# Performance work log

Measured on AMD Instinct MI355X. Metric: run time of the kernel, lower is better.

The kernel has to match this reference:

```python
import jax, jax.numpy as jnp
import numpy as np

FEATURE_MAPS = [8, 4, 2, 1]
BOXES_PER_LOC = [4, 6, 6, 4]
IMAGE_SIZE = 128
DECODED_SIZE = 64
Z_WHAT = 64
CHANNELS = [64, 256, 128, 64, 32, 16, 3]  # conv-transpose pyramid 1x1 -> 64x64
BATCH = 4
EMPTY_CONST = -1000.0
N_LOC = sum(f * f for f in FEATURE_MAPS)            # 85
N_BOX = sum(f * f * b for f, b in zip(FEATURE_MAPS, BOXES_PER_LOC))  # 380


def _recon_indices():
    # Decoder.reconstruction_indices: expand per-location latents to per-box.
    idx, last = [], 0
    for fm, bpl in zip(FEATURE_MAPS, BOXES_PER_LOC):
        for i in range(fm * fm):
            idx.append(np.full(bpl, last + i, dtype=np.int32))
        last += fm * fm
    return np.concatenate(idx)


def setup_inputs() -> dict:
    key = jax.random.key(0)
    ks = jax.random.split(key, 16)
    inp = {
        'z_what': jax.random.normal(ks[0], (BATCH, N_LOC, Z_WHAT), jnp.float32),
        'z_where': jax.random.uniform(ks[1], (BATCH, N_BOX, 4), jnp.float32),
        'z_present': jax.random.randint(ks[2], (BATCH, N_BOX, 1), 0, 2).astype(jnp.int32),
        'z_depth': jax.random.normal(ks[3], (BATCH, N_LOC, 1), jnp.float32),
    }
    for i, (cin, cout) in enumerate(zip(CHANNELS[:-1], CHANNELS[1:])):
        inp[f'w{i}'] = jax.random.normal(ks[4 + i], (2, 2, cin, cout), jnp.float32) / np.sqrt(4.0 * cin)
        inp[f'b{i}'] = jnp.zeros((cout,), jnp.float32)
    return inp


def _what_decoder(z_flat, params):
    # (N, Z) -> (N, 3, 64, 64): stack of stride-2 kernel-2 conv transposes.
    x = z_flat[:, :, None, None]
    n = len(params)
    for i, (w, b) in enumerate(params):
        x = jax.lax.conv_transpose(x, w, strides=(2, 2), padding='VALID',
                                   dimension_numbers=('NCHW', 'HWIO', 'NCHW'))
        x = x + b[None, :, None, None]
        x = jax.nn.sigmoid(x) if i == n - 1 else jax.nn.relu(x)
    return x


def _sample_bilinear(img, px, py):
    # img (3, D, D); px/py (S,) pixel coords along cols/rows; zero outside.
    D = DECODED_SIZE
    x0 = jnp.floor(px)
    y0 = jnp.floor(py)
    wx = px - x0
    wy = py - y0

    def gather(yi, xi):
        vy = (yi >= 0) & (yi <= D - 1)
        vx = (xi >= 0) & (xi <= D - 1)
        yc = jnp.clip(yi.astype(jnp.int32), 0, D - 1)
        xc = jnp.clip(xi.astype(jnp.int32), 0, D - 1)
        vals = img[:, yc[:, None], xc[None, :]]  # (3, S, S)
        return vals * (vy[:, None] & vx[None, :]).astype(img.dtype)

    g00 = gather(y0, x0)
    g01 = gather(y0, x0 + 1)
    g10 = gather(y0 + 1, x0)
    g11 = gather(y0 + 1, x0 + 1)
    wyc = wy[None, :, None]
    wxc = wx[None, None, :]
    return (g00 * (1 - wyc) * (1 - wxc) + g01 * (1 - wyc) * wxc
            + g10 * wyc * (1 - wxc) + g11 * wyc * wxc)


def _where_stn(imgs, z_where):
    # Paste each decoded glyph into an IMAGE_SIZE canvas at box (cx, cy, w, h).
    S, D = IMAGE_SIZE, DECODED_SIZE
    cx, cy, w, h = (z_where[:, i] for i in range(4))
    sx = jnp.maximum(w, 1e-5)
    sy = jnp.maximum(h, 1e-5)
    out = jnp.linspace(-1.0, 1.0, S)
    xin = (out[None, :] - (2 * cx - 1)[:, None]) / sx[:, None]  # (N, S)
    yin = (out[None, :] - (2 * cy - 1)[:, None]) / sy[:, None]
    px = (xin + 1) * (D - 1) / 2
    py = (yin + 1) * (D - 1) / 2
    return jax.vmap(_sample_bilinear)(imgs, px, py)  # (N, 3, S, S)


def reference(z_what, z_where, z_present, z_depth, w0, b0, w1, b1, w2, b2, w3, b3, w4, b4, w5, b5):
    params = [(w0, b0), (w1, b1), (w2, b2), (w3, b3), (w4, b4), (w5, b5)]
    idx = jnp.asarray(_recon_indices())
    zw = jnp.take(z_what, idx, axis=1)   # (B, N_BOX, Z)
    zd = jnp.take(z_depth, idx, axis=1)  # (B, N_BOX, 1)
    B = zw.shape[0]
    decoded = _what_decoder(zw.reshape(B * N_BOX, Z_WHAT), params)
    transformed = _where_stn(decoded, z_where.reshape(B * N_BOX, 4))
    recon = transformed.reshape(B, N_BOX, 3, IMAGE_SIZE, IMAGE_SIZE)
    depths = jnp.where(z_present[..., 0] == 1, zd[..., 0], EMPTY_CONST)  # (B, N_BOX)
    weights = jax.nn.softmax(depths, axis=1)
    return jnp.einsum('bn,bnchw->bchw', weights, recon)
```

## Files before the change

kernel.cpp:

```cpp
#include <hip/hip_runtime.h>
#include <hip/hip_bf16.h>

#define NBOX  380
#define NLOCS 85
#define NINST 340
#define SPLIT 2

__device__ __forceinline__ int loc_of_box(int n) {
    if (n < 256) return n >> 2;
    if (n < 352) return 64 + (n - 256) / 6;
    if (n < 376) return 80 + (n - 352) / 6;
    return 84;
}

__device__ void box_params_dev(int b, const float* __restrict__ zwhere,
    const int* __restrict__ zpresent, const float* __restrict__ zdepth,
    float* wgt, float* sxs, float* oxs, float* sys, float* oys,
    int* binst, int* rect, int* cidx, int* cnt, float* sm)
{
    float* sd  = sm;
    float* red = sm + 384;
    const int tid = threadIdx.x;

    if (tid < NBOX) {
        int loc = loc_of_box(tid);
        sd[tid] = (zpresent[b * NBOX + tid] == 1) ? zdepth[b * NLOCS + loc] : -1000.0f;
    }
    __syncthreads();

    float m = (tid < NBOX) ? sd[tid] : -1e30f;
    red[tid] = m; __syncthreads();
    for (int s = 256; s > 0; s >>= 1) {
        if (tid < s) red[tid] = fmaxf(red[tid], red[tid + s]);
        __syncthreads();
    }
    m = red[0]; __syncthreads();

    float sum = (tid < NBOX) ? expf(sd[tid] - m) : 0.f;
    red[tid] = sum; __syncthreads();
    for (int s = 256; s > 0; s >>= 1) {
        if (tid < s) red[tid] += red[tid + s];
        __syncthreads();
    }
    float inv = 1.0f / red[0];
    __syncthreads();

    if (tid < NBOX) {
        int g = b * NBOX + tid;
        float wv = expf(sd[tid] - m) * inv;
        wgt[g] = wv;
        float cx = zwhere[g * 4 + 0], cy = zwhere[g * 4 + 1];
        float w  = zwhere[g * 4 + 2], h  = zwhere[g * 4 + 3];
        float isx = 1.0f / fmaxf(w, 1e-5f);
        float isy = 1.0f / fmaxf(h, 1e-5f);
        float sxv = isx * (63.0f / 127.0f);
        float oxv = 31.5f * (1.0f - 2.0f * cx * isx);
        float syv = isy * (63.0f / 127.0f);
        float oyv = 31.5f * (1.0f - 2.0f * cy * isy);
        sxs[g] = sxv; oxs[g] = oxv; sys[g] = syv; oys[g] = oyv;
        binst[g] = b * NLOCS + loc_of_box(tid);
        int wlo = min(127, max(0, (int)floorf((-1.0f - oxv) / sxv)));
        int whi = max(0, min(127, (int)ceilf((64.0f - oxv) / sxv)));
        int hlo = min(127, max(0, (int)floorf((-1.0f - oyv) / syv)));
        int hhi = max(0, min(127, (int)ceilf((64.0f - oyv) / syv)));
        rect[g] = wlo | (whi << 8) | (hlo << 16) | (hhi << 24);
        sd[tid] = wv;
    }
    __syncthreads();

    if (tid < 64) {
        int base = 0;
        for (int c = 0; c < 6; ++c) {
            int n = c * 64 + tid;
            bool p = (n < NBOX) && (sd[n] > 0.0f);
            unsigned long long mask = __ballot(p);
            int pos = __popcll(mask & ((1ull << tid) - 1ull));
            if (p) cidx[b * NBOX + base + pos] = n;
            base += __popcll(mask);
        }
        if (tid == 0) cnt[b] = base;
    }
}

__global__ __launch_bounds__(512, 2) void decode_fused_k(
    const float* __restrict__ z_what,
    const float* __restrict__ W0, const float* __restrict__ B0,
    const float* __restrict__ W1, const float* __restrict__ B1,
    const float* __restrict__ W2, const float* __restrict__ B2,
    const float* __restrict__ W3, const float* __restrict__ B3,
    const float* __restrict__ W4, const float* __restrict__ B4,
    const float* __restrict__ W5, const float* __restrict__ B5,
    const float* __restrict__ z_where, const int* __restrict__ z_present,
    const float* __restrict__ z_depth,
    float* __restrict__ wgt, float* __restrict__ sxs, float* __restrict__ oxs,
    float* __restrict__ sys, float* __restrict__ oys, int* __restrict__ binst,
    int* __restrict__ rect, int* __restrict__ cidx, int* __restrict__ cnt,
    float* __restrict__ dec)
{
    __shared__ __align__(16) float sm[13312];

    const int bid = blockIdx.x;
    if (bid >= SPLIT * NINST) {
        box_params_dev(bid - SPLIT * NINST, z_where, z_present, z_depth,
                       wgt, sxs, oxs, sys, oys, binst, rect, cidx, cnt, sm);
        return;
    }
    const int s    = bid / NINST;
    const int inst = bid - s * NINST;

    float* s_x = sm;
    float* aL0 = sm + 64;
    float* aL1 = sm + 576;
    float* aL2 = sm + 1600;
    float* aL4 = sm;
    float* aL3 = sm + 8704;

    const int tid = threadIdx.x;

    if (tid < 64) s_x[tid] = z_what[inst * 64 + tid];
    __syncthreads();

    {
        const int c0 = tid & 255;
        const int j0 = tid >> 8;
        const int ft = 3 - (2 * s + j0);
        const float* wp = W0 + (size_t)ft * 64 * 256 + c0;
        float a = 0.f;
        #pragma unroll 8
        for (int k = 0; k < 64; ++k)
            a = fmaf(s_x[k], wp[k * 256], a);
        aL0[j0 * 256 + c0] = fmaxf(a + B0[c0], 0.f);
    }
    __syncthreads();

    {
        const int c1 = tid & 127;
        const int x1 = tid >> 7;
        const int j = x1 >> 1, dj = x1 & 1;
        const float* wA = W1 + (size_t)(3 - dj) * 256 * 128 + c1;
        const float* wB = W1 + (size_t)(1 - dj) * 256 * 128 + c1;
        const float* xp = aL0 + j * 256;
        float a0 = 0.f, a1 = 0.f;
        #pragma unroll 4
        for (int q = 0; q < 64; ++q) {
            float4 xq = *(const float4*)&xp[q * 4];
            a0 = fmaf(xq.x, wA[(q*4+0)*128], a0); a1 = fmaf(xq.x, wB[(q*4+0)*128], a1);
            a0 = fmaf(xq.y, wA[(q*4+1)*128], a0); a1 = fmaf(xq.y, wB[(q*4+1)*128], a1);
            a0 = fmaf(xq.z, wA[(q*4+2)*128], a0); a1 = fmaf(xq.z, wB[(q*4+2)*128], a1);
            a0 = fmaf(xq.w, wA[(q*4+3)*128], a0); a1 = fmaf(xq.w, wB[(q*4+3)*128], a1);
        }
        float bb = B1[c1];
        aL1[(0 * 4 + x1) * 128 + c1] = fmaxf(a0 + bb, 0.f);
        aL1[(1 * 4 + x1) * 128 + c1] = fmaxf(a1 + bb, 0.f);
    }
    __syncthreads();

    {
        const int c2 = tid & 63;
        const int x2 = tid >> 6;
        const int j = x2 >> 1, dj = x2 & 1;
        const float* wA = W2 + (size_t)(3 - dj) * 128 * 64 + c2;
        const float* wB = W2 + (size_t)(1 - dj) * 128 * 64 + c2;
        const float* xp0 = aL1 + (0 * 4 + j) * 128;
        const float* xp1 = aL1 + (1 * 4 + j) * 128;
        float a00 = 0.f, a01 = 0.f, a10 = 0.f, a11 = 0.f;
        #pragma unroll 4
        for (int q = 0; q < 32; ++q) {
            float4 x0 = *(const float4*)&xp0[q * 4];
            float4 x1 = *(const float4*)&xp1[q * 4];
            #pragma unroll
            for (int kk = 0; kk < 4; ++kk) {
                int k = q * 4 + kk;
                float xa = (kk==0)?x0.x:(kk==1)?x0.y:(kk==2)?x0.z:x0.w;
                float xb = (kk==0)?x1.x:(kk==1)?x1.y:(kk==2)?x1.z:x1.w;
                float wa = wA[k * 64], wb = wB[k * 64];
                a00 = fmaf(xa, wa, a00); a01 = fmaf(xa, wb, a01);
                a10 = fmaf(xb, wa, a10); a11 = fmaf(xb, wb, a11);
            }
        }
        float bb = B2[c2];
        aL2[(0 * 8 + x2) * 64 + c2] = fmaxf(a00 + bb, 0.f);
        aL2[(1 * 8 + x2) * 64 + c2] = fmaxf(a01 + bb, 0.f);
        aL2[(2 * 8 + x2) * 64 + c2] = fmaxf(a10 + bb, 0.f);
        aL2[(3 * 8 + x2) * 64 + c2] = fmaxf(a11 + bb, 0.f);
    }
    __syncthreads();

    {
        const int c3 = tid & 31;
        const int x3 = tid >> 5;
        const int j = x3 >> 1, dj = x3 & 1;
        const float* wA = W3 + (size_t)(3 - dj) * 64 * 32 + c3;
        const float* wB = W3 + (size_t)(1 - dj) * 64 * 32 + c3;
        float accA[4], accB[4];
        #pragma unroll
        for (int il = 0; il < 4; ++il) { accA[il] = 0.f; accB[il] = 0.f; }
        #pragma unroll
        for (int q = 0; q < 16; ++q) {
            float4 xr[4];
            #pragma unroll
            for (int il = 0; il < 4; ++il)
                xr[il] = *(const float4*)&aL2[(il * 8 + j) * 64 + q * 4];
            #pragma unroll
            for (int kk = 0; kk < 4; ++kk) {
                int k = q * 4 + kk;
                float wa = wA[k * 32], wb = wB[k * 32];
                #pragma unroll
                for (int il = 0; il < 4; ++il) {
                    float xv = (kk==0)?xr[il].x:(kk==1)?xr[il].y:(kk==2)?xr[il].z:xr[il].w;
                    accA[il] = fmaf(xv, wa, accA[il]);
                    accB[il] = fmaf(xv, wb, accB[il]);
                }
            }
        }
        float bb = B3[c3];
        #pragma unroll
        for (int il = 0; il < 4; ++il) {
            aL3[((2 * il + 0) * 16 + x3) * 36 + c3] = fmaxf(accA[il] + bb, 0.f);
            aL3[((2 * il + 1) * 16 + x3) * 36 + c3] = fmaxf(accB[il] + bb, 0.f);
        }
    }
    __syncthreads();

    {
        const int c4 = tid & 15;
        const int x4 = tid >> 4;
        const int j = x4 >> 1, dj = x4 & 1;
        const float* wA = W4 + (size_t)(3 - dj) * 32 * 16 + c4;
        const float* wB = W4 + (size_t)(1 - dj) * 32 * 16 + c4;
        float accA[8], accB[8];
        #pragma unroll
        for (int il = 0; il < 8; ++il) { accA[il] = 0.f; accB[il] = 0.f; }
        #pragma unroll
        for (int q = 0; q < 8; ++q) {
            float4 xr[8];
            #pragma unroll
            for (int il = 0; il < 8; ++il)
                xr[il] = *(const float4*)&aL3[(il * 16 + j) * 36 + q * 4];
            #pragma unroll
            for (int kk = 0; kk < 4; ++kk) {
                int k = q * 4 + kk;
                float wa = wA[k * 16], wb = wB[k * 16];
                #pragma unroll
                for (int il = 0; il < 8; ++il) {
                    float xv = (kk==0)?xr[il].x:(kk==1)?xr[il].y:(kk==2)?xr[il].z:xr[il].w;
                    accA[il] = fmaf(xv, wa, accA[il]);
                    accB[il] = fmaf(xv, wb, accB[il]);
                }
            }
        }
        float bb = B4[c4];
        #pragma unroll
        for (int il = 0; il < 8; ++il) {
            aL4[((2 * il + 0) * 32 + x4) * 17 + c4] = fmaxf(accA[il] + bb, 0.f);
            aL4[((2 * il + 1) * 32 + x4) * 17 + c4] = fmaxf(accB[il] + bb, 0.f);
        }
    }
    __syncthreads();

    {
        const int x5 = tid & 63;
        const int g  = tid >> 6;
        const int j = x5 >> 1, dj = x5 & 1, di = g & 1;
        const int ft = 3 - (2 * di + dj);
        const float* wp = W5 + ft * 48;
        float ar[4][3];
        #pragma unroll
        for (int r = 0; r < 4; ++r) { ar[r][0] = B5[0]; ar[r][1] = B5[1]; ar[r][2] = B5[2]; }
        #pragma unroll
        for (int k = 0; k < 16; ++k) {
            float w0 = wp[k * 3 + 0], w1 = wp[k * 3 + 1], w2 = wp[k * 3 + 2];
            #pragma unroll
            for (int r = 0; r < 4; ++r) {
                int y5l = g + 8 * r;
                float xv = aL4[((y5l >> 1) * 32 + j) * 17 + k];
                ar[r][0] = fmaf(xv, w0, ar[r][0]);
                ar[r][1] = fmaf(xv, w1, ar[r][1]);
                ar[r][2] = fmaf(xv, w2, ar[r][2]);
            }
        }
        #pragma unroll
        for (int r = 0; r < 4; ++r) {
            int y5l = g + 8 * r;
            float v0 = 1.0f / (1.0f + expf(-ar[r][0]));
            float v1 = 1.0f / (1.0f + expf(-ar[r][1]));
            float v2 = 1.0f / (1.0f + expf(-ar[r][2]));
            float* dp = dec + (size_t)inst * 12288
                      + (size_t)((32 * s + y5l) * 64 + x5) * 3;
            dp[0] = v0; dp[1] = v1; dp[2] = v2;
        }
    }
}

__global__ __launch_bounds__(1024) void composite_k(
    const float* __restrict__ dec, const float* __restrict__ wgt,
    const float* __restrict__ sxs, const float* __restrict__ oxs,
    const float* __restrict__ sys, const float* __restrict__ oys,
    const int* __restrict__ binst, const int* __restrict__ rect,
    const int* __restrict__ cidx, const int* __restrict__ cnt,
    float* __restrict__ out)
{
    __shared__ float pls[8][128][3];

    int b = blockIdx.x >> 7, tile = blockIdx.x & 127;
    int tx0 = (tile & 7) << 4, ty0 = (tile >> 3) << 3;
    int s = threadIdx.x >> 7, px = threadIdx.x & 127;
    int lx = px & 15, ly = px >> 4;
    int w = tx0 + lx, h = ty0 + ly;

    int nb = cnt[b];
    int lo = (nb * s) >> 3, hi = (nb * (s + 1)) >> 3;

    float fw = (float)w, fh = (float)h;
    float a0 = 0.f, a1 = 0.f, a2 = 0.f;
    for (int q = lo; q < hi; ++q) {
        int n = cidx[b * NBOX + q];
        int rc = rect[b * NBOX + n];
        int wlo = rc & 255, whi = (rc >> 8) & 255;
        int hlo = (rc >> 16) & 255, hhi = (rc >> 24) & 255;
        if (whi < tx0 || wlo > tx0 + 15 || hhi < ty0 || hlo > ty0 + 7) continue;
        int g = b * NBOX + n;
        float wg = wgt[g];
        float pxx = fmaf(fw, sxs[g], oxs[g]);
        float pyy = fmaf(fh, sys[g], oys[g]);
        float x0 = floorf(pxx), y0 = floorf(pyy);
        if (x0 < -1.0f || x0 > 63.0f || y0 < -1.0f || y0 > 63.0f) continue;
        float wx = pxx - x0, wy = pyy - y0;
        int ix = (int)x0, iy = (int)y0;
        int x0c = max(ix, 0), x1c = min(ix + 1, 63);
        int y0c = max(iy, 0), y1c = min(iy + 1, 63);
        float m00 = (ix >= 0 && iy >= 0) ? 1.f : 0.f;
        float m01 = (ix + 1 <= 63 && iy >= 0) ? 1.f : 0.f;
        float m10 = (ix >= 0 && iy + 1 <= 63) ? 1.f : 0.f;
        float m11 = (ix + 1 <= 63 && iy + 1 <= 63) ? 1.f : 0.f;
        float w00 = (1.f - wy) * (1.f - wx) * m00;
        float w01 = (1.f - wy) * wx * m01;
        float w10 = wy * (1.f - wx) * m10;
        float w11 = wy * wx * m11;
        const float* img = dec + (size_t)binst[g] * 12288;
        int b00 = (y0c * 64 + x0c) * 3, b01 = (y0c * 64 + x1c) * 3;
        int b10 = (y1c * 64 + x0c) * 3, b11 = (y1c * 64 + x1c) * 3;
        a0 += wg * (w00 * img[b00]   + w01 * img[b01]   + w10 * img[b10]   + w11 * img[b11]);
        a1 += wg * (w00 * img[b00+1] + w01 * img[b01+1] + w10 * img[b10+1] + w11 * img[b11+1]);
        a2 += wg * (w00 * img[b00+2] + w01 * img[b01+2] + w10 * img[b10+2] + w11 * img[b11+2]);
    }
    pls[s][px][0] = a0; pls[s][px][1] = a1; pls[s][px][2] = a2;
    __syncthreads();

    if (threadIdx.x < 384) {
        int c = threadIdx.x >> 7, p2 = threadIdx.x & 127;
        float v = 0.f;
        #pragma unroll
        for (int t = 0; t < 8; ++t) v += pls[t][p2][c];
        int h2 = ty0 + (p2 >> 4), w2 = tx0 + (p2 & 15);
        out[((b * 3 + c) * 128 + h2) * 128 + w2] = v;
    }
}

extern "C" void kernel_launch(void* const* d_in, const int* in_sizes, int n_in,
                              void* d_out, int out_size, void* d_ws, size_t ws_size,
                              hipStream_t stream)
{
    const float* z_what    = (const float*)d_in[0];
    const float* z_where   = (const float*)d_in[1];
    const int*   z_present = (const int*)  d_in[2];
    const float* z_depth   = (const float*)d_in[3];

    char* ws = (char*)d_ws;
    float* dec = (float*)ws;
    float* P   = (float*)(ws + 16711680);
    float* wgt = P,        *sxs = P + 1520, *oxs = P + 2 * 1520;
    float* sys = P + 3 * 1520, *oys = P + 4 * 1520;
    int* binst = (int*)(P + 5 * 1520);
    int* rect  = binst + 1520;
    int* cidx  = binst + 2 * 1520;
    int* cnt   = binst + 3 * 1520;

    decode_fused_k<<<dim3(SPLIT * NINST + 4), dim3(512), 0, stream>>>(
        z_what,
        (const float*)d_in[4],  (const float*)d_in[5],
        (const float*)d_in[6],  (const float*)d_in[7],
        (const float*)d_in[8],  (const float*)d_in[9],
        (const float*)d_in[10], (const float*)d_in[11],
        (const float*)d_in[12], (const float*)d_in[13],
        (const float*)d_in[14], (const float*)d_in[15],
        z_where, z_present, z_depth,
        wgt, sxs, oxs, sys, oys, binst, rect, cidx, cnt,
        dec);

    composite_k<<<dim3(512), dim3(1024), 0, stream>>>(
        dec, wgt, sxs, oxs, sys, oys, binst, rect, cidx, cnt, (float*)d_out);
}
```

Measured before the change: 92.47 us.

## Decode two batch instances per block sharing weight loads, chunk last layers

Each decode block now processes two instances (same location, different batch entries) together, so every weight value loaded from global memory feeds two accumulators, halving weight traffic per instance. The grid shrinks from 680 to 340 decode blocks. Layers 4 and 5 are computed in four row chunks so shared memory fits both instances, and layer-5 weights are held in registers. This trades extra register pressure, more barriers, and fewer blocks (which may reduce occupancy and parallelism on a large GPU) for less redundant weight loading.

```diff
diff --git a/kernel.cpp b/kernel.cpp
--- a/kernel.cpp
+++ b/kernel.cpp
@@ -4,13 +4,16 @@
 #define NBOX  380
 #define NLOCS 85
 #define NINST 340
-#define SPLIT 2
 
 __device__ __forceinline__ int loc_of_box(int n) {
     if (n < 256) return n >> 2;
     if (n < 352) return 64 + (n - 256) / 6;
     if (n < 376) return 80 + (n - 352) / 6;
     return 84;
+}
+
+__device__ __forceinline__ float f4e(const float4& v, int kk) {
+    return (kk == 0) ? v.x : (kk == 1) ? v.y : (kk == 2) ? v.z : v.w;
 }
 
 __device__ void box_params_dev(int b, const float* __restrict__ zwhere,
@@ -97,198 +100,251 @@
     int* __restrict__ rect, int* __restrict__ cidx, int* __restrict__ cnt,
     float* __restrict__ dec)
 {
-    __shared__ __align__(16) float sm[13312];
+    __shared__ __align__(16) float sm[15360];
 
     const int bid = blockIdx.x;
-    if (bid >= SPLIT * NINST) {
-        box_params_dev(bid - SPLIT * NINST, z_where, z_present, z_depth,
+    if (bid >= NINST) {
+        box_params_dev(bid - NINST, z_where, z_present, z_depth,
                        wgt, sxs, oxs, sys, oys, binst, rect, cidx, cnt, sm);
         return;
     }
-    const int s    = bid / NINST;
-    const int inst = bid - s * NINST;
-
-    float* s_x = sm;
-    float* aL0 = sm + 64;
-    float* aL1 = sm + 576;
-    float* aL2 = sm + 1600;
-    float* aL4 = sm;
-    float* aL3 = sm + 8704;
+    const int loc = bid % 85;
+    const int r2  = bid / 85;
+    const int bp  = r2 & 1, s = r2 >> 1;
+    const int inst0 = (2 * bp + 0) * 85 + loc;
+    const int inst1 = (2 * bp + 1) * 85 + loc;
 
     const int tid = threadIdx.x;
 
-    if (tid < 64) s_x[tid] = z_what[inst * 64 + tid];
+    if (tid < 128) {
+        int q = tid >> 6, l = tid & 63;
+        sm[q * 7680 + 3584 + l] = z_what[(q ? inst1 : inst0) * 64 + l];
+    }
     __syncthreads();
 
     {
-        const int c0 = tid & 255;
-        const int j0 = tid >> 8;
+        const int c0 = tid & 255, j0 = tid >> 8;
         const int ft = 3 - (2 * s + j0);
         const float* wp = W0 + (size_t)ft * 64 * 256 + c0;
-        float a = 0.f;
+        const float* x0 = sm + 3584;
+        const float* x1 = sm + 7680 + 3584;
+        float a0 = 0.f, a1 = 0.f;
         #pragma unroll 8
-        for (int k = 0; k < 64; ++k)
-            a = fmaf(s_x[k], wp[k * 256], a);
-        aL0[j0 * 256 + c0] = fmaxf(a + B0[c0], 0.f);
+        for (int k = 0; k < 64; ++k) {
+            float w = wp[k * 256];
+            a0 = fmaf(x0[k], w, a0);
+            a1 = fmaf(x1[k], w, a1);
+        }
+        float bb = B0[c0];
+        sm[j0 * 256 + c0]        = fmaxf(a0 + bb, 0.f);
+        sm[7680 + j0 * 256 + c0] = fmaxf(a1 + bb, 0.f);
     }
     __syncthreads();
 
     {
-        const int c1 = tid & 127;
-        const int x1 = tid >> 7;
-        const int j = x1 >> 1, dj = x1 & 1;
-        const float* wA = W1 + (size_t)(3 - dj) * 256 * 128 + c1;
-        const float* wB = W1 + (size_t)(1 - dj) * 256 * 128 + c1;
-        const float* xp = aL0 + j * 256;
-        float a0 = 0.f, a1 = 0.f;
+        const int c1 = tid & 127, t = tid >> 7;
+        const int di = t >> 1, dj = t & 1, ft = 3 - t;
+        const float* wp = W1 + (size_t)ft * 256 * 128 + c1;
+        float aA0 = 0.f, aA1 = 0.f, aB0 = 0.f, aB1 = 0.f;
         #pragma unroll 4
-        for (int q = 0; q < 64; ++q) {
-            float4 xq = *(const float4*)&xp[q * 4];
-            a0 = fmaf(xq.x, wA[(q*4+0)*128], a0); a1 = fmaf(xq.x, wB[(q*4+0)*128], a1);
-            a0 = fmaf(xq.y, wA[(q*4+1)*128], a0); a1 = fmaf(xq.y, wB[(q*4+1)*128], a1);
-            a0 = fmaf(xq.z, wA[(q*4+2)*128], a0); a1 = fmaf(xq.z, wB[(q*4+2)*128], a1);
-            a0 = fmaf(xq.w, wA[(q*4+3)*128], a0); a1 = fmaf(xq.w, wB[(q*4+3)*128], a1);
+        for (int kq = 0; kq < 64; ++kq) {
+            int k0 = kq * 4;
+            float4 vA0 = *(const float4*)&sm[0 * 256 + k0];
+            float4 vA1 = *(const float4*)&sm[1 * 256 + k0];
+            float4 vB0 = *(const float4*)&sm[7680 + 0 * 256 + k0];
+            float4 vB1 = *(const float4*)&sm[7680 + 1 * 256 + k0];
+            #pragma unroll
+            for (int kk = 0; kk < 4; ++kk) {
+                float w = wp[(k0 + kk) * 128];
+                aA0 = fmaf(f4e(vA0, kk), w, aA0);
+                aA1 = fmaf(f4e(vA1, kk), w, aA1);
+                aB0 = fmaf(f4e(vB0, kk), w, aB0);
+                aB1 = fmaf(f4e(vB1, kk), w, aB1);
+            }
         }
         float bb = B1[c1];
-        aL1[(0 * 4 + x1) * 128 + c1] = fmaxf(a0 + bb, 0.f);
-        aL1[(1 * 4 + x1) * 128 + c1] = fmaxf(a1 + bb, 0.f);
+        int o0 = (di * 4 + 0 + dj) * 128 + c1;
+        int o1 = (di * 4 + 2 + dj) * 128 + c1;
+        sm[512 + o0]        = fmaxf(aA0 + bb, 0.f);
+        sm[512 + o1]        = fmaxf(aA1 + bb, 0.f);
+        sm[7680 + 512 + o0] = fmaxf(aB0 + bb, 0.f);
+        sm[7680 + 512 + o1] = fmaxf(aB1 + bb, 0.f);
     }
     __syncthreads();
 
     {
-        const int c2 = tid & 63;
-        const int x2 = tid >> 6;
+        const int c2 = tid & 63, x2 = tid >> 6;
         const int j = x2 >> 1, dj = x2 & 1;
         const float* wA = W2 + (size_t)(3 - dj) * 128 * 64 + c2;
         const float* wB = W2 + (size_t)(1 - dj) * 128 * 64 + c2;
-        const float* xp0 = aL1 + (0 * 4 + j) * 128;
-        const float* xp1 = aL1 + (1 * 4 + j) * 128;
-        float a00 = 0.f, a01 = 0.f, a10 = 0.f, a11 = 0.f;
-        #pragma unroll 4
-        for (int q = 0; q < 32; ++q) {
-            float4 x0 = *(const float4*)&xp0[q * 4];
-            float4 x1 = *(const float4*)&xp1[q * 4];
+        float acc[2][2][2];
+        #pragma unroll
+        for (int q = 0; q < 2; ++q)
+            #pragma unroll
+            for (int il = 0; il < 2; ++il) { acc[q][il][0] = 0.f; acc[q][il][1] = 0.f; }
+        #pragma unroll 2
+        for (int kq = 0; kq < 32; ++kq) {
+            int k0 = kq * 4;
+            float4 xr[2][2];
+            #pragma unroll
+            for (int q = 0; q < 2; ++q)
+                #pragma unroll
+                for (int il = 0; il < 2; ++il)
+                    xr[q][il] = *(const float4*)&sm[q * 7680 + 512 + (il * 4 + j) * 128 + k0];
             #pragma unroll
             for (int kk = 0; kk < 4; ++kk) {
-                int k = q * 4 + kk;
-                float xa = (kk==0)?x0.x:(kk==1)?x0.y:(kk==2)?x0.z:x0.w;
-                float xb = (kk==0)?x1.x:(kk==1)?x1.y:(kk==2)?x1.z:x1.w;
-                float wa = wA[k * 64], wb = wB[k * 64];
-                a00 = fmaf(xa, wa, a00); a01 = fmaf(xa, wb, a01);
-                a10 = fmaf(xb, wa, a10); a11 = fmaf(xb, wb, a11);
+                float wa = wA[(k0 + kk) * 64], wb = wB[(k0 + kk) * 64];
+                #pragma unroll
+                for (int q = 0; q < 2; ++q)
+                    #pragma unroll
+                    for (int il = 0; il < 2; ++il) {
+                        float e = f4e(xr[q][il], kk);
+                        acc[q][il][0] = fmaf(e, wa, acc[q][il][0]);
+                        acc[q][il][1] = fmaf(e, wb, acc[q][il][1]);
+                    }
             }
         }
         float bb = B2[c2];
-        aL2[(0 * 8 + x2) * 64 + c2] = fmaxf(a00 + bb, 0.f);
-        aL2[(1 * 8 + x2) * 64 + c2] = fmaxf(a01 + bb, 0.f);
-        aL2[(2 * 8 + x2) * 64 + c2] = fmaxf(a10 + bb, 0.f);
-        aL2[(3 * 8 + x2) * 64 + c2] = fmaxf(a11 + bb, 0.f);
+        #pragma unroll
+        for (int q = 0; q < 2; ++q)
+            #pragma unroll
+            for (int il = 0; il < 2; ++il)
+                #pragma unroll
+                for (int di = 0; di < 2; ++di)
+                    sm[q * 7680 + 1536 + ((2 * il + di) * 8 + x2) * 64 + c2] =
+                        fmaxf(acc[q][il][di] + bb, 0.f);
     }
     __syncthreads();
 
     {
-        const int c3 = tid & 31;
-        const int x3 = tid >> 5;
+        const int c3 = tid & 31, x3 = tid >> 5;
         const int j = x3 >> 1, dj = x3 & 1;
         const float* wA = W3 + (size_t)(3 - dj) * 64 * 32 + c3;
         const float* wB = W3 + (size_t)(1 - dj) * 64 * 32 + c3;
-        float accA[4], accB[4];
+        float acc[2][4][2];
         #pragma unroll
-        for (int il = 0; il < 4; ++il) { accA[il] = 0.f; accB[il] = 0.f; }
-        #pragma unroll
-        for (int q = 0; q < 16; ++q) {
-            float4 xr[4];
-            #pragma unroll
-            for (int il = 0; il < 4; ++il)
-                xr[il] = *(const float4*)&aL2[(il * 8 + j) * 64 + q * 4];
+        for (int q = 0; q < 2; ++q)
+            #pragma unroll
+            for (int il = 0; il < 4; ++il) { acc[q][il][0] = 0.f; acc[q][il][1] = 0.f; }
+        #pragma unroll 2
+        for (int kq = 0; kq < 16; ++kq) {
+            int k0 = kq * 4;
+            float4 xr[2][4];
+            #pragma unroll
+            for (int q = 0; q < 2; ++q)
+                #pragma unroll
+                for (int il = 0; il < 4; ++il)
+                    xr[q][il] = *(const float4*)&sm[q * 7680 + 1536 + (il * 8 + j) * 64 + k0];
             #pragma unroll
             for (int kk = 0; kk < 4; ++kk) {
-                int k = q * 4 + kk;
-                float wa = wA[k * 32], wb = wB[k * 32];
-                #pragma unroll
-                for (int il = 0; il < 4; ++il) {
-                    float xv = (kk==0)?xr[il].x:(kk==1)?xr[il].y:(kk==2)?xr[il].z:xr[il].w;
-                    accA[il] = fmaf(xv, wa, accA[il]);
-                    accB[il] = fmaf(xv, wb, accB[il]);
-                }
+                float wa = wA[(k0 + kk) * 32], wb = wB[(k0 + kk) * 32];
+                #pragma unroll
+                for (int q = 0; q < 2; ++q)
+                    #pragma unroll
+                    for (int il = 0; il < 4; ++il) {
+                        float e = f4e(xr[q][il], kk);
+                        acc[q][il][0] = fmaf(e, wa, acc[q][il][0]);
+                        acc[q][il][1] = fmaf(e, wb, acc[q][il][1]);
+                    }
             }
         }
         float bb = B3[c3];
         #pragma unroll
-        for (int il = 0; il < 4; ++il) {
-            aL3[((2 * il + 0) * 16 + x3) * 36 + c3] = fmaxf(accA[il] + bb, 0.f);
-            aL3[((2 * il + 1) * 16 + x3) * 36 + c3] = fmaxf(accB[il] + bb, 0.f);
-        }
-    }
-    __syncthreads();
-
-    {
-        const int c4 = tid & 15;
-        const int x4 = tid >> 4;
-        const int j = x4 >> 1, dj = x4 & 1;
-        const float* wA = W4 + (size_t)(3 - dj) * 32 * 16 + c4;
-        const float* wB = W4 + (size_t)(1 - dj) * 32 * 16 + c4;
-        float accA[8], accB[8];
-        #pragma unroll
-        for (int il = 0; il < 8; ++il) { accA[il] = 0.f; accB[il] = 0.f; }
-        #pragma unroll
-        for (int q = 0; q < 8; ++q) {
-            float4 xr[8];
-            #pragma unroll
-            for (int il = 0; il < 8; ++il)
-                xr[il] = *(const float4*)&aL3[(il * 16 + j) * 36 + q * 4];
-            #pragma unroll
-            for (int kk = 0; kk < 4; ++kk) {
-                int k = q * 4 + kk;
-                float wa = wA[k * 16], wb = wB[k * 16];
-                #pragma unroll
-                for (int il = 0; il < 8; ++il) {
-                    float xv = (kk==0)?xr[il].x:(kk==1)?xr[il].y:(kk==2)?xr[il].z:xr[il].w;
-                    accA[il] = fmaf(xv, wa, accA[il]);
-                    accB[il] = fmaf(xv, wb, accB[il]);
+        for (int q = 0; q < 2; ++q)
+            #pragma unroll
+            for (int il = 0; il < 4; ++il)
+                #pragma unroll
+                for (int di = 0; di < 2; ++di)
+                    sm[q * 7680 + 3584 + ((2 * il + di) * 16 + x3) * 32 + c3] =
+                        fmaxf(acc[q][il][di] + bb, 0.f);
+    }
+    __syncthreads();
+
+    const float b50 = B5[0], b51 = B5[1], b52 = B5[2];
+    const int x5 = tid & 63, g5 = tid >> 6;
+    const int dj5 = x5 & 1, di5 = g5 & 1;
+    const int ft5 = 3 - (2 * di5 + dj5);
+    float w5r[16][3];
+    #pragma unroll
+    for (int k = 0; k < 16; ++k) {
+        w5r[k][0] = W5[(ft5 * 16 + k) * 3 + 0];
+        w5r[k][1] = W5[(ft5 * 16 + k) * 3 + 1];
+        w5r[k][2] = W5[(ft5 * 16 + k) * 3 + 2];
+    }
+
+    for (int c = 0; c < 4; ++c) {
+        {
+            const int c4 = tid & 15, x4 = tid >> 4;
+            const int j = x4 >> 1, dj = x4 & 1;
+            const float* wA = W4 + (size_t)(3 - dj) * 32 * 16 + c4;
+            const float* wB = W4 + (size_t)(1 - dj) * 32 * 16 + c4;
+            float acc[2][2][2];
+            #pragma unroll
+            for (int q = 0; q < 2; ++q)
+                #pragma unroll
+                for (int il = 0; il < 2; ++il) { acc[q][il][0] = 0.f; acc[q][il][1] = 0.f; }
+            #pragma unroll
+            for (int kq = 0; kq < 8; ++kq) {
+                int k0 = kq * 4;
+                float4 xr[2][2];
+                #pragma unroll
+                for (int q = 0; q < 2; ++q)
+                    #pragma unroll
+                    for (int il = 0; il < 2; ++il)
+                        xr[q][il] = *(const float4*)
+                            &sm[q * 7680 + 3584 + ((2 * c + il) * 16 + j) * 32 + k0];
+                #pragma unroll
+                for (int kk = 0; kk < 4; ++kk) {
+                    float wa = wA[(k0 + kk) * 16], wb = wB[(k0 + kk) * 16];
+                    #pragma unroll
+                    for (int q = 0; q < 2; ++q)
+                        #pragma unroll
+                        for (int il = 0; il < 2; ++il) {
+                            float e = f4e(xr[q][il], kk);
+                            acc[q][il][0] = fmaf(e, wa, acc[q][il][0]);
+                            acc[q][il][1] = fmaf(e, wb, acc[q][il][1]);
+                        }
                 }
             }
-        }
-        float bb = B4[c4];
-        #pragma unroll
-        for (int il = 0; il < 8; ++il) {
-            aL4[((2 * il + 0) * 32 + x4) * 17 + c4] = fmaxf(accA[il] + bb, 0.f);
-            aL4[((2 * il + 1) * 32 + x4) * 17 + c4] = fmaxf(accB[il] + bb, 0.f);
-        }
-    }
-    __syncthreads();
-
-    {
-        const int x5 = tid & 63;
-        const int g  = tid >> 6;
-        const int j = x5 >> 1, dj = x5 & 1, di = g & 1;
-        const int ft = 3 - (2 * di + dj);
-        const float* wp = W5 + ft * 48;
-        float ar[4][3];
-        #pragma unroll
-        for (int r = 0; r < 4; ++r) { ar[r][0] = B5[0]; ar[r][1] = B5[1]; ar[r][2] = B5[2]; }
-        #pragma unroll
-        for (int k = 0; k < 16; ++k) {
-            float w0 = wp[k * 3 + 0], w1 = wp[k * 3 + 1], w2 = wp[k * 3 + 2];
-            #pragma unroll
-            for (int r = 0; r < 4; ++r) {
-                int y5l = g + 8 * r;
-                float xv = aL4[((y5l >> 1) * 32 + j) * 17 + k];
-                ar[r][0] = fmaf(xv, w0, ar[r][0]);
-                ar[r][1] = fmaf(xv, w1, ar[r][1]);
-                ar[r][2] = fmaf(xv, w2, ar[r][2]);
-            }
-        }
-        #pragma unroll
-        for (int r = 0; r < 4; ++r) {
-            int y5l = g + 8 * r;
-            float v0 = 1.0f / (1.0f + expf(-ar[r][0]));
-            float v1 = 1.0f / (1.0f + expf(-ar[r][1]));
-            float v2 = 1.0f / (1.0f + expf(-ar[r][2]));
-            float* dp = dec + (size_t)inst * 12288
-                      + (size_t)((32 * s + y5l) * 64 + x5) * 3;
-            dp[0] = v0; dp[1] = v1; dp[2] = v2;
-        }
+            float bb = B4[c4];
+            #pragma unroll
+            for (int q = 0; q < 2; ++q)
+                #pragma unroll
+                for (int il = 0; il < 2; ++il)
+                    #pragma unroll
+                    for (int di = 0; di < 2; ++di)
+                        sm[q * 7680 + ((2 * il + di) * 32 + x4) * 17 + c4] =
+                            fmaxf(acc[q][il][di] + bb, 0.f);
+        }
+        __syncthreads();
+        {
+            const int jl = x5 >> 1;
+            const int lr = g5 >> 1;
+            float a[2][3];
+            #pragma unroll
+            for (int q = 0; q < 2; ++q) { a[q][0] = b50; a[q][1] = b51; a[q][2] = b52; }
+            #pragma unroll
+            for (int k = 0; k < 16; ++k) {
+                #pragma unroll
+                for (int q = 0; q < 2; ++q) {
+                    float xv = sm[q * 7680 + (lr * 32 + jl) * 17 + k];
+                    a[q][0] = fmaf(xv, w5r[k][0], a[q][0]);
+                    a[q][1] = fmaf(xv, w5r[k][1], a[q][1]);
+                    a[q][2] = fmaf(xv, w5r[k][2], a[q][2]);
+                }
+            }
+            int row = 32 * s + 8 * c + g5;
+            #pragma unroll
+            for (int q = 0; q < 2; ++q) {
+                float v0 = 1.0f / (1.0f + expf(-a[q][0]));
+                float v1 = 1.0f / (1.0f + expf(-a[q][1]));
+                float v2 = 1.0f / (1.0f + expf(-a[q][2]));
+                float* dp = dec + (size_t)(q ? inst1 : inst0) * 12288
+                          + (size_t)(row * 64 + x5) * 3;
+                dp[0] = v0; dp[1] = v1; dp[2] = v2;
+            }
+        }
+        __syncthreads();
     }
 }
 
@@ -376,7 +432,7 @@
     int* cidx  = binst + 2 * 1520;
     int* cnt   = binst + 3 * 1520;
 
-    decode_fused_k<<<dim3(SPLIT * NINST + 4), dim3(512), 0, stream>>>(
+    decode_fused_k<<<dim3(NINST + 4), dim3(512), 0, stream>>>(
         z_what,
         (const float*)d_in[4],  (const float*)d_in[5],
         (const float*)d_in[6],  (const float*)d_in[7],
```

Result: no change. 93.61 us (+1.2%).
